# Optimization experiments

Measured on AMD Instinct MI355X. Metric: run time of the kernel, lower is better.

The kernel has to match this reference:

```python
import jax, jax.numpy as jnp
import numpy as np

H = 2048
K_SRC = (H * H) // 4  # exact nonzero count of mask_src (fixed in setup_inputs)
K_TAR = (H * H) // 4  # exact nonzero count of mask_tar
NBINS = 256


def de_norm(x):
    return jnp.clip((x + 1.0) / 2.0, 0.0, 1.0)


def cal_hist_cdf(vals):
    # vals: [3, K] float in [0, 255]. torch.histc(bins=256, min=0, max=256)
    # has unit-width bins -> bin index = floor(v). Returns cumulative pdf [3, 256].
    idx = jnp.clip(vals.astype(jnp.int32), 0, NBINS - 1)
    flat = (idx + jnp.arange(3, dtype=jnp.int32)[:, None] * NBINS).ravel()
    hist = jnp.bincount(flat, length=3 * NBINS).reshape(3, NBINS).astype(vals.dtype)
    pdf = hist / hist.sum(axis=1, keepdims=True)
    return jnp.cumsum(pdf, axis=1)


def cal_trans(dst_cdf, ref_cdf):
    # Faithful to PSGAN cal_trans(ref=dst_cdf, adj=ref_cdf):
    # table[i] = first j in [1,255] with ref_cdf[j-1] <= dst_cdf[i] <= ref_cdf[j],
    # else i; table[255] = 255. First valid j equals searchsorted-left (clipped).
    i = jnp.arange(NBINS)
    j = jnp.clip(jnp.searchsorted(ref_cdf, dst_cdf, side='left'), 1, NBINS - 1)
    valid = (ref_cdf[j - 1] <= dst_cdf) & (dst_cdf <= ref_cdf[j])
    table = jnp.where(valid, j, i)
    return table.at[NBINS - 1].set(NBINS - 1)


def setup_inputs():
    key = jax.random.key(0)
    k1, k2 = jax.random.split(key)
    rng = np.random.default_rng(0)

    def make_mask(K):
        m = np.zeros(H * H, np.float32)
        m[rng.permutation(H * H)[:K]] = 1.0
        return jnp.asarray(m.reshape(1, 1, H, H))

    return {
        "input_data": jax.random.normal(k1, (1, 3, H, H), jnp.float32),
        "target_data": jax.random.normal(k2, (1, 3, H, H), jnp.float32),
        "mask_src": make_mask(K_SRC),
        "mask_tar": make_mask(K_TAR),
    }


def reference(input_data, target_data, mask_src, mask_tar):
    m_src = mask_src[0, 0]  # [H, H]
    m_tar = mask_tar[0, 0]
    # nonzero() returns row-major (y, x) index pairs, same as torch
    ys, xs = jnp.nonzero(m_src, size=K_SRC)
    yt, xt = jnp.nonzero(m_tar, size=K_TAR)

    inp = de_norm(input_data)[0] * 255.0   # [3, H, H]
    tar = de_norm(target_data)[0] * 255.0
    input_masked = inp * m_src[None]
    target_masked = tar * m_tar[None]

    dst_align = input_masked[:, ys, xs]    # [3, K_SRC]
    ref_align = target_masked[:, yt, xt]   # [3, K_TAR]

    cdf_dst = cal_hist_cdf(dst_align)
    cdf_ref = cal_hist_cdf(ref_align)
    tables = jax.vmap(cal_trans)(cdf_dst, cdf_ref)  # [3, 256]

    # remap: tables[c][int(dst_align[c,k])] (int() truncation, values >= 0)
    bins = jnp.clip(dst_align.astype(jnp.int32), 0, NBINS - 1)
    mapped = jnp.take_along_axis(tables, bins, axis=1).astype(input_masked.dtype)

    # scatter matched values back into the masked input image; detached in torch
    input_match = jax.lax.stop_gradient(input_masked.at[:, ys, xs].set(mapped))
    return jnp.mean(jnp.abs(input_masked - input_match))
```

## Files before the change

kernel.cpp:

```cpp
#include <hip/hip_runtime.h>
#include <hip/hip_bf16.h>

#define HDIM 2048
#define HH (HDIM * HDIM)
#define NBINS 256
#define KCNT 1048576.0f
#define TOTAL_ELEMS 12582912.0

#define NBLK 2048
#define FRAC_SCALE 4096.0f
#define FRAC_INV   (1.0 / 4096.0)

#define ROW_DWORDS 1536
#define ROW_BYTES  6144
#define TAIL_BYTES (1536 * sizeof(int) + 768 * sizeof(int))
#define ROWS_PER_CHUNK 32

__global__ void __launch_bounds__(256, 8) hist_kernel(
        const float* __restrict__ inp,
        const float* __restrict__ tar,
        const float* __restrict__ msrc,
        const float* __restrict__ mtar,
        unsigned int* __restrict__ parts) {
    __shared__ unsigned int hs[3 * NBINS];
    __shared__ unsigned int ht[3 * NBINS];
    for (int i = threadIdx.x; i < 3 * NBINS; i += blockDim.x) {
        hs[i] = 0u;
        ht[i] = 0u;
    }
    __syncthreads();

    int nf[6] = {0, 0, 0, 0, 0, 0};

    const int stride = NBLK * 256;
    const int n4 = HH / 4;
    for (int p4 = blockIdx.x * 256 + threadIdx.x; p4 < n4; p4 += stride) {
        const float4 ms4 = ((const float4*)msrc)[p4];
        const float4 mt4 = ((const float4*)mtar)[p4];
        float mk[4] = {ms4.x, ms4.y, ms4.z, ms4.w};
        float tk[4] = {mt4.x, mt4.y, mt4.z, mt4.w};
        #pragma unroll
        for (int c = 0; c < 3; ++c) {
            const float4 v4 = ((const float4*)(inp + (size_t)c * HH))[p4];
            const float4 w4 = ((const float4*)(tar + (size_t)c * HH))[p4];
            const float vv[4] = {v4.x, v4.y, v4.z, v4.w};
            const float ww[4] = {w4.x, w4.y, w4.z, w4.w};
            #pragma unroll
            for (int k = 0; k < 4; ++k) {
                {
                    const bool on = (mk[k] != 0.0f);
                    const float vr   = (vv[k] + 1.0f) * 0.5f;
                    const float v255 = fminf(fmaxf(vr, 0.0f), 1.0f) * 255.0f;
                    const bool hi = (v255 >= 255.0f);
                    const bool lo = (v255 <= 0.0f);
                    nf[c] += (int)(on && hi);
                    if (on && !lo && !hi) {
                        const int b = (int)v255;
                        const unsigned fx =
                            (unsigned)((v255 - (float)b) * FRAC_SCALE);
                        atomicAdd(&hs[c * NBINS + b], (1u << 20) | fx);
                    }
                }
                {
                    const bool on = (tk[k] != 0.0f);
                    const float vr   = (ww[k] + 1.0f) * 0.5f;
                    const float v255 = fminf(fmaxf(vr, 0.0f), 1.0f) * 255.0f;
                    const bool hi = (v255 >= 255.0f);
                    const bool lo = (v255 <= 0.0f);
                    nf[3 + c] += (int)(on && hi);
                    if (on && !lo && !hi)
                        atomicAdd(&ht[c * NBINS + (int)v255], 1u);
                }
            }
        }
    }

    const int lane = threadIdx.x & 63;
    #pragma unroll
    for (int j = 0; j < 6; ++j) {
        int f = nf[j];
        #pragma unroll
        for (int off = 32; off > 0; off >>= 1)
            f += __shfl_down(f, off, 64);
        if (lane == 0 && f) {
            if (j < 3) atomicAdd(&hs[j * NBINS + NBINS - 1], ((unsigned)f) << 20);
            else       atomicAdd(&ht[(j - 3) * NBINS + NBINS - 1], (unsigned)f);
        }
    }
    __syncthreads();

    unsigned int* row = parts + (size_t)blockIdx.x * ROW_DWORDS;
    for (int i = threadIdx.x; i < ROW_DWORDS; i += blockDim.x)
        row[i] = (i < 3 * NBINS) ? hs[i] : ht[i - 3 * NBINS];
}

__global__ void reduce_kernel(const unsigned int* __restrict__ parts, int nblk,
                              int* __restrict__ counts,
                              int* __restrict__ fracsI) {
    const int j = blockIdx.x * blockDim.x + threadIdx.x;
    if (j >= ROW_DWORDS) return;
    int w0 = blockIdx.y * ROWS_PER_CHUNK;
    int w1 = w0 + ROWS_PER_CHUNK;
    if (w1 > nblk) w1 = nblk;
    if (w0 >= w1) return;

    if (j < 768) {
        unsigned cnt = 0, fr = 0;
        for (int w = w0; w < w1; ++w) {
            unsigned p = parts[(size_t)w * ROW_DWORDS + j];
            cnt += p >> 20;
            fr  += p & 0xFFFFFu;
        }
        if (cnt) atomicAdd(&counts[j], (int)cnt);
        if (fr)  atomicAdd(&fracsI[j], (int)fr);
    } else {
        unsigned cnt = 0;
        for (int w = w0; w < w1; ++w)
            cnt += parts[(size_t)w * ROW_DWORDS + j];
        if (cnt) atomicAdd(&counts[j], (int)cnt);
    }
}

__global__ void final_kernel(const int* __restrict__ counts,
                             const int* __restrict__ fracsI,
                             float* __restrict__ out) {
    __shared__ float cdf[6][NBINS];
    __shared__ int   lcnt[6 * NBINS];
    __shared__ double red[12];
    const int tid = threadIdx.x;
    lcnt[tid]       = counts[tid];
    lcnt[tid + 768] = counts[tid + 768];
    __syncthreads();

    if (tid < 6) {
        int tot = 0;
        for (int i = 1; i < NBINS; ++i) tot += lcnt[tid * NBINS + i];
        lcnt[tid * NBINS + 0] = (1 << 20) - tot;
        float run = 0.0f;
        for (int i = 0; i < NBINS; ++i) {
            run += (float)lcnt[tid * NBINS + i] * (1.0f / KCNT);
            cdf[tid][i] = run;
        }
    }
    __syncthreads();

    const int c = tid >> 8, b = tid & (NBINS - 1);
    const float d = cdf[c][b];
    const float* r = cdf[3 + c];
    int lo = 0, hi = NBINS;
    while (lo < hi) {
        int mid = (lo + hi) >> 1;
        if (r[mid] < d) lo = mid + 1; else hi = mid;
    }
    int j = lo;
    if (j < 1) j = 1;
    if (j > NBINS - 1) j = NBINS - 1;
    bool valid = (r[j - 1] <= d) && (d <= r[j]);
    int t = valid ? j : b;
    if (b == NBINS - 1) t = NBINS - 1;

    const int n = lcnt[c * NBINS + b];
    const double s = (double)n * (double)b
                   + (double)fracsI[c * NBINS + b] * FRAC_INV;
    double contrib = (t <= b) ? (s - (double)n * (double)t)
                              : ((double)n * (double)t - s);

    #pragma unroll
    for (int off = 32; off > 0; off >>= 1)
        contrib += __shfl_down(contrib, off, 64);
    const int wave = tid >> 6, lane = tid & 63;
    if (lane == 0) red[wave] = contrib;
    __syncthreads();
    if (tid == 0) {
        double tot = 0.0;
        for (int w = 0; w < 12; ++w) tot += red[w];
        out[0] = (float)(tot / TOTAL_ELEMS);
    }
}

extern "C" void kernel_launch(void* const* d_in, const int* in_sizes, int n_in,
                              void* d_out, int out_size, void* d_ws, size_t ws_size,
                              hipStream_t stream) {
    const float* inp  = (const float*)d_in[0];
    const float* tar  = (const float*)d_in[1];
    const float* msrc = (const float*)d_in[2];
    const float* mtar = (const float*)d_in[3];
    float* out = (float*)d_out;

    char* ws = (char*)d_ws;
    unsigned int* parts  = (unsigned int*)ws;
    int*          counts = (int*)(ws + (size_t)NBLK * ROW_BYTES);
    int*          fracsI = (int*)(ws + (size_t)NBLK * ROW_BYTES + 1536 * sizeof(int));

    hipMemsetAsync((void*)counts, 0, TAIL_BYTES, stream);

    const int nchunks = (NBLK + ROWS_PER_CHUNK - 1) / ROWS_PER_CHUNK;
    dim3 rgrid((ROW_DWORDS + 255) / 256, nchunks);

    hist_kernel<<<NBLK, 256, 0, stream>>>(inp, tar, msrc, mtar, parts);
    reduce_kernel<<<rgrid, 256, 0, stream>>>(parts, NBLK, counts, fracsI);
    final_kernel<<<1, 3 * NBINS, 0, stream>>>(counts, fracsI, out);
}
```

Baseline: 50.41 us.

## Fuse reduce and final kernels with last-block ticket, drop memset, halve grid

Removes the memset by having block 0 of the histogram kernel zero the accumulators and ticket. The reduce and final kernels are merged into one, where the last block to finish (found with an atomic ticket) computes the CDFs, the transfer tables and the loss. The histogram grid is halved to 1024 blocks, which means fewer partial rows to reduce but more work per block. The aim is to cut launch count and reduction traffic, at the cost of a serial tail in a single 256-thread block.

```diff
diff --git a/kernel.cpp b/kernel.cpp
--- a/kernel.cpp
+++ b/kernel.cpp
@@ -7,13 +7,13 @@
 #define KCNT 1048576.0f
 #define TOTAL_ELEMS 12582912.0
 
-#define NBLK 2048
+#define NBLK 1024
 #define FRAC_SCALE 4096.0f
 #define FRAC_INV   (1.0 / 4096.0)
 
 #define ROW_DWORDS 1536
 #define ROW_BYTES  6144
-#define TAIL_BYTES (1536 * sizeof(int) + 768 * sizeof(int))
+#define TAIL_WORDS 2305
 #define ROWS_PER_CHUNK 32
 
 __global__ void __launch_bounds__(256, 8) hist_kernel(
@@ -21,13 +21,17 @@
         const float* __restrict__ tar,
         const float* __restrict__ msrc,
         const float* __restrict__ mtar,
-        unsigned int* __restrict__ parts) {
+        unsigned int* __restrict__ parts,
+        unsigned int* __restrict__ tail) {
     __shared__ unsigned int hs[3 * NBINS];
     __shared__ unsigned int ht[3 * NBINS];
     for (int i = threadIdx.x; i < 3 * NBINS; i += blockDim.x) {
         hs[i] = 0u;
         ht[i] = 0u;
     }
+    if (blockIdx.x == 0)
+        for (int i = threadIdx.x; i < TAIL_WORDS; i += blockDim.x)
+            tail[i] = 0u;
     __syncthreads();
 
     int nf[6] = {0, 0, 0, 0, 0, 0};
@@ -37,8 +41,8 @@
     for (int p4 = blockIdx.x * 256 + threadIdx.x; p4 < n4; p4 += stride) {
         const float4 ms4 = ((const float4*)msrc)[p4];
         const float4 mt4 = ((const float4*)mtar)[p4];
-        float mk[4] = {ms4.x, ms4.y, ms4.z, ms4.w};
-        float tk[4] = {mt4.x, mt4.y, mt4.z, mt4.w};
+        const float mk[4] = {ms4.x, ms4.y, ms4.z, ms4.w};
+        const float tk[4] = {mt4.x, mt4.y, mt4.z, mt4.w};
         #pragma unroll
         for (int c = 0; c < 3; ++c) {
             const float4 v4 = ((const float4*)(inp + (size_t)c * HH))[p4];
@@ -94,20 +98,19 @@
         row[i] = (i < 3 * NBINS) ? hs[i] : ht[i - 3 * NBINS];
 }
 
-__global__ void reduce_kernel(const unsigned int* __restrict__ parts, int nblk,
-                              int* __restrict__ counts,
-                              int* __restrict__ fracsI) {
+__global__ void reduce_final_kernel(const unsigned int* __restrict__ parts,
+                                    int* __restrict__ counts,
+                                    int* __restrict__ fracsI,
+                                    unsigned int* __restrict__ ticket,
+                                    float* __restrict__ out) {
     const int j = blockIdx.x * blockDim.x + threadIdx.x;
-    if (j >= ROW_DWORDS) return;
-    int w0 = blockIdx.y * ROWS_PER_CHUNK;
-    int w1 = w0 + ROWS_PER_CHUNK;
-    if (w1 > nblk) w1 = nblk;
-    if (w0 >= w1) return;
+    const int w0 = blockIdx.y * ROWS_PER_CHUNK;
+    const int w1 = w0 + ROWS_PER_CHUNK;
 
     if (j < 768) {
         unsigned cnt = 0, fr = 0;
         for (int w = w0; w < w1; ++w) {
-            unsigned p = parts[(size_t)w * ROW_DWORDS + j];
+            const unsigned p = parts[(size_t)w * ROW_DWORDS + j];
             cnt += p >> 20;
             fr  += p & 0xFFFFFu;
         }
@@ -119,63 +122,72 @@
             cnt += parts[(size_t)w * ROW_DWORDS + j];
         if (cnt) atomicAdd(&counts[j], (int)cnt);
     }
-}
-
-__global__ void final_kernel(const int* __restrict__ counts,
-                             const int* __restrict__ fracsI,
-                             float* __restrict__ out) {
+
+    __threadfence();
+    __shared__ int isLast;
+    if (threadIdx.x == 0) {
+        const unsigned total = gridDim.x * gridDim.y;
+        isLast = (atomicAdd(ticket, 1u) == total - 1u);
+    }
+    __syncthreads();
+    if (!isLast) return;
+
+    __shared__ int   lcnt[6 * NBINS];
+    __shared__ int   lfr[3 * NBINS];
     __shared__ float cdf[6][NBINS];
-    __shared__ int   lcnt[6 * NBINS];
-    __shared__ double red[12];
-    const int tid = threadIdx.x;
-    lcnt[tid]       = counts[tid];
-    lcnt[tid + 768] = counts[tid + 768];
-    __syncthreads();
-
-    if (tid < 6) {
+    __shared__ double red[4];
+    for (int i = threadIdx.x; i < 6 * NBINS; i += blockDim.x)
+        lcnt[i] = atomicAdd(&counts[i], 0);
+    for (int i = threadIdx.x; i < 3 * NBINS; i += blockDim.x)
+        lfr[i] = atomicAdd(&fracsI[i], 0);
+    __syncthreads();
+
+    if (threadIdx.x < 6) {
+        const int c = threadIdx.x;
         int tot = 0;
-        for (int i = 1; i < NBINS; ++i) tot += lcnt[tid * NBINS + i];
-        lcnt[tid * NBINS + 0] = (1 << 20) - tot;
+        for (int i = 1; i < NBINS; ++i) tot += lcnt[c * NBINS + i];
+        lcnt[c * NBINS + 0] = (1 << 20) - tot;
         float run = 0.0f;
         for (int i = 0; i < NBINS; ++i) {
-            run += (float)lcnt[tid * NBINS + i] * (1.0f / KCNT);
-            cdf[tid][i] = run;
-        }
-    }
-    __syncthreads();
-
-    const int c = tid >> 8, b = tid & (NBINS - 1);
-    const float d = cdf[c][b];
-    const float* r = cdf[3 + c];
-    int lo = 0, hi = NBINS;
-    while (lo < hi) {
-        int mid = (lo + hi) >> 1;
-        if (r[mid] < d) lo = mid + 1; else hi = mid;
-    }
-    int j = lo;
-    if (j < 1) j = 1;
-    if (j > NBINS - 1) j = NBINS - 1;
-    bool valid = (r[j - 1] <= d) && (d <= r[j]);
-    int t = valid ? j : b;
-    if (b == NBINS - 1) t = NBINS - 1;
-
-    const int n = lcnt[c * NBINS + b];
-    const double s = (double)n * (double)b
-                   + (double)fracsI[c * NBINS + b] * FRAC_INV;
-    double contrib = (t <= b) ? (s - (double)n * (double)t)
-                              : ((double)n * (double)t - s);
+            run += (float)lcnt[c * NBINS + i] * (1.0f / KCNT);
+            cdf[c][i] = run;
+        }
+    }
+    __syncthreads();
+
+    double acc = 0.0;
+    #pragma unroll
+    for (int ci = 0; ci < 3; ++ci) {
+        const int c = ci, b = threadIdx.x;
+        const float d = cdf[c][b];
+        const float* r = cdf[3 + c];
+        int lo = 0, hi = NBINS;
+        while (lo < hi) {
+            const int mid = (lo + hi) >> 1;
+            if (r[mid] < d) lo = mid + 1; else hi = mid;
+        }
+        int jj = lo;
+        if (jj < 1) jj = 1;
+        if (jj > NBINS - 1) jj = NBINS - 1;
+        const bool valid = (r[jj - 1] <= d) && (d <= r[jj]);
+        int t = valid ? jj : b;
+        if (b == NBINS - 1) t = NBINS - 1;
+
+        const int n = lcnt[c * NBINS + b];
+        const double s = (double)n * (double)b
+                       + (double)lfr[c * NBINS + b] * FRAC_INV;
+        acc += (t <= b) ? (s - (double)n * (double)t)
+                        : ((double)n * (double)t - s);
+    }
 
     #pragma unroll
     for (int off = 32; off > 0; off >>= 1)
-        contrib += __shfl_down(contrib, off, 64);
-    const int wave = tid >> 6, lane = tid & 63;
-    if (lane == 0) red[wave] = contrib;
-    __syncthreads();
-    if (tid == 0) {
-        double tot = 0.0;
-        for (int w = 0; w < 12; ++w) tot += red[w];
-        out[0] = (float)(tot / TOTAL_ELEMS);
-    }
+        acc += __shfl_down(acc, off, 64);
+    const int wave = threadIdx.x >> 6, lane = threadIdx.x & 63;
+    if (lane == 0) red[wave] = acc;
+    __syncthreads();
+    if (threadIdx.x == 0)
+        out[0] = (float)((red[0] + red[1] + red[2] + red[3]) / TOTAL_ELEMS);
 }
 
 extern "C" void kernel_launch(void* const* d_in, const int* in_sizes, int n_in,
@@ -189,15 +201,14 @@
 
     char* ws = (char*)d_ws;
     unsigned int* parts  = (unsigned int*)ws;
-    int*          counts = (int*)(ws + (size_t)NBLK * ROW_BYTES);
-    int*          fracsI = (int*)(ws + (size_t)NBLK * ROW_BYTES + 1536 * sizeof(int));
-
-    hipMemsetAsync((void*)counts, 0, TAIL_BYTES, stream);
-
-    const int nchunks = (NBLK + ROWS_PER_CHUNK - 1) / ROWS_PER_CHUNK;
-    dim3 rgrid((ROW_DWORDS + 255) / 256, nchunks);
-
-    hist_kernel<<<NBLK, 256, 0, stream>>>(inp, tar, msrc, mtar, parts);
-    reduce_kernel<<<rgrid, 256, 0, stream>>>(parts, NBLK, counts, fracsI);
-    final_kernel<<<1, 3 * NBINS, 0, stream>>>(counts, fracsI, out);
+    unsigned int* tail   = (unsigned int*)(ws + (size_t)NBLK * ROW_BYTES);
+    int*          counts = (int*)tail;
+    int*          fracsI = (int*)(tail + 1536);
+    unsigned int* ticket = tail + 2304;
+
+    hist_kernel<<<NBLK, 256, 0, stream>>>(inp, tar, msrc, mtar, parts, tail);
+
+    dim3 rgrid(ROW_DWORDS / 256, NBLK / ROWS_PER_CHUNK);
+    reduce_final_kernel<<<rgrid, 256, 0, stream>>>(parts, counts, fracsI,
+                                                   ticket, out);
 }
```

Result: slower. 56.30 us (+11.7%).

## Halve hist grid, use nontemporal loads, zero accumulators in-kernel instead of memset

Applied to the files above, without the earlier changes.

Reduces the histogram grid from 2048 to 1024 blocks, which halves the partial-histogram rows that must be written and later reduced. Image loads switch to nontemporal builtins so the streamed data does not pollute the caches. The hipMemsetAsync is removed and block 0 of the histogram kernel zeroes the accumulators instead, saving a launch. The reduce kernel drops its bounds checks because the grid now divides evenly. With fewer blocks, each thread handles more elements, which may lower the latency hiding available.

```diff
diff --git a/kernel.cpp b/kernel.cpp
--- a/kernel.cpp
+++ b/kernel.cpp
@@ -7,27 +7,37 @@
 #define KCNT 1048576.0f
 #define TOTAL_ELEMS 12582912.0
 
-#define NBLK 2048
+#define NBLK 1024
 #define FRAC_SCALE 4096.0f
 #define FRAC_INV   (1.0 / 4096.0)
 
 #define ROW_DWORDS 1536
 #define ROW_BYTES  6144
-#define TAIL_BYTES (1536 * sizeof(int) + 768 * sizeof(int))
+#define TAIL_WORDS 2304
 #define ROWS_PER_CHUNK 32
+
+typedef float floatx4 __attribute__((ext_vector_type(4)));
+
+__device__ __forceinline__ floatx4 nt_load4(const float* p) {
+    return __builtin_nontemporal_load((const floatx4*)p);
+}
 
 __global__ void __launch_bounds__(256, 8) hist_kernel(
         const float* __restrict__ inp,
         const float* __restrict__ tar,
         const float* __restrict__ msrc,
         const float* __restrict__ mtar,
-        unsigned int* __restrict__ parts) {
+        unsigned int* __restrict__ parts,
+        unsigned int* __restrict__ tail) {
     __shared__ unsigned int hs[3 * NBINS];
     __shared__ unsigned int ht[3 * NBINS];
     for (int i = threadIdx.x; i < 3 * NBINS; i += blockDim.x) {
         hs[i] = 0u;
         ht[i] = 0u;
     }
+    if (blockIdx.x == 0)
+        for (int i = threadIdx.x; i < TAIL_WORDS; i += blockDim.x)
+            tail[i] = 0u;
     __syncthreads();
 
     int nf[6] = {0, 0, 0, 0, 0, 0};
@@ -37,19 +47,17 @@
     for (int p4 = blockIdx.x * 256 + threadIdx.x; p4 < n4; p4 += stride) {
         const float4 ms4 = ((const float4*)msrc)[p4];
         const float4 mt4 = ((const float4*)mtar)[p4];
-        float mk[4] = {ms4.x, ms4.y, ms4.z, ms4.w};
-        float tk[4] = {mt4.x, mt4.y, mt4.z, mt4.w};
+        const float mk[4] = {ms4.x, ms4.y, ms4.z, ms4.w};
+        const float tk[4] = {mt4.x, mt4.y, mt4.z, mt4.w};
         #pragma unroll
         for (int c = 0; c < 3; ++c) {
-            const float4 v4 = ((const float4*)(inp + (size_t)c * HH))[p4];
-            const float4 w4 = ((const float4*)(tar + (size_t)c * HH))[p4];
-            const float vv[4] = {v4.x, v4.y, v4.z, v4.w};
-            const float ww[4] = {w4.x, w4.y, w4.z, w4.w};
+            const floatx4 v4 = nt_load4(inp + (size_t)c * HH + (size_t)p4 * 4);
+            const floatx4 w4 = nt_load4(tar + (size_t)c * HH + (size_t)p4 * 4);
             #pragma unroll
             for (int k = 0; k < 4; ++k) {
                 {
                     const bool on = (mk[k] != 0.0f);
-                    const float vr   = (vv[k] + 1.0f) * 0.5f;
+                    const float vr   = (v4[k] + 1.0f) * 0.5f;
                     const float v255 = fminf(fmaxf(vr, 0.0f), 1.0f) * 255.0f;
                     const bool hi = (v255 >= 255.0f);
                     const bool lo = (v255 <= 0.0f);
@@ -63,7 +71,7 @@
                 }
                 {
                     const bool on = (tk[k] != 0.0f);
-                    const float vr   = (ww[k] + 1.0f) * 0.5f;
+                    const float vr   = (w4[k] + 1.0f) * 0.5f;
                     const float v255 = fminf(fmaxf(vr, 0.0f), 1.0f) * 255.0f;
                     const bool hi = (v255 >= 255.0f);
                     const bool lo = (v255 <= 0.0f);
@@ -94,20 +102,17 @@
         row[i] = (i < 3 * NBINS) ? hs[i] : ht[i - 3 * NBINS];
 }
 
-__global__ void reduce_kernel(const unsigned int* __restrict__ parts, int nblk,
+__global__ void reduce_kernel(const unsigned int* __restrict__ parts,
                               int* __restrict__ counts,
                               int* __restrict__ fracsI) {
     const int j = blockIdx.x * blockDim.x + threadIdx.x;
-    if (j >= ROW_DWORDS) return;
-    int w0 = blockIdx.y * ROWS_PER_CHUNK;
-    int w1 = w0 + ROWS_PER_CHUNK;
-    if (w1 > nblk) w1 = nblk;
-    if (w0 >= w1) return;
+    const int w0 = blockIdx.y * ROWS_PER_CHUNK;
+    const int w1 = w0 + ROWS_PER_CHUNK;
 
     if (j < 768) {
         unsigned cnt = 0, fr = 0;
         for (int w = w0; w < w1; ++w) {
-            unsigned p = parts[(size_t)w * ROW_DWORDS + j];
+            const unsigned p = parts[(size_t)w * ROW_DWORDS + j];
             cnt += p >> 20;
             fr  += p & 0xFFFFFu;
         }
@@ -189,15 +194,13 @@
 
     char* ws = (char*)d_ws;
     unsigned int* parts  = (unsigned int*)ws;
-    int*          counts = (int*)(ws + (size_t)NBLK * ROW_BYTES);
-    int*          fracsI = (int*)(ws + (size_t)NBLK * ROW_BYTES + 1536 * sizeof(int));
-
-    hipMemsetAsync((void*)counts, 0, TAIL_BYTES, stream);
-
-    const int nchunks = (NBLK + ROWS_PER_CHUNK - 1) / ROWS_PER_CHUNK;
-    dim3 rgrid((ROW_DWORDS + 255) / 256, nchunks);
-
-    hist_kernel<<<NBLK, 256, 0, stream>>>(inp, tar, msrc, mtar, parts);
-    reduce_kernel<<<rgrid, 256, 0, stream>>>(parts, NBLK, counts, fracsI);
+    unsigned int* tail   = (unsigned int*)(ws + (size_t)NBLK * ROW_BYTES);
+    int*          counts = (int*)tail;
+    int*          fracsI = (int*)(tail + 1536);
+
+    hist_kernel<<<NBLK, 256, 0, stream>>>(inp, tar, msrc, mtar, parts, tail);
+
+    dim3 rgrid(ROW_DWORDS / 256, NBLK / ROWS_PER_CHUNK);
+    reduce_kernel<<<rgrid, 256, 0, stream>>>(parts, counts, fracsI);
     final_kernel<<<1, 3 * NBINS, 0, stream>>>(counts, fracsI, out);
 }
```

Result: faster. 44.67 us (-11.4%).
